# Optimization experiments

Hardware: AMD Instinct MI355X
Metric: run time of the kernel (lower is better)

## Reference

```python
import jax, jax.numpy as jnp
import numpy as np

K = 10           # polynomial order
N = 100000       # num nodes
E = 3200000      # num edges
F_IN = 512       # input feature dim
C = 64           # num classes


def setup_inputs() -> dict:
    key = jax.random.key(0)
    ks = jax.random.split(key, 6)
    x = jax.random.normal(ks[0], (N, F_IN), dtype=jnp.float32)
    edge_index = jax.random.randint(ks[1], (2, E), 0, N, dtype=jnp.int64)
    W = jax.random.normal(ks[2], (F_IN, C), dtype=jnp.float32) * (1.0 / np.sqrt(F_IN))
    b = jax.random.normal(ks[3], (C,), dtype=jnp.float32) * 0.01
    lap_coefs = jax.random.uniform(ks[4], (K + 1,), dtype=jnp.float32)
    mf_weights = jax.random.uniform(ks[5], (1, K + 1, C), dtype=jnp.float32)
    return {"x": x, "edge_index": edge_index, "W": W, "b": b,
            "lap_coefs": lap_coefs, "mf_weights": mf_weights}


def reference(x, edge_index, W, b, lap_coefs, mf_weights):
    row, col = edge_index[0], edge_index[1]
    # GCN norm without self-loops: deg over targets (col), sym normalization
    ones = jnp.ones((row.shape[0],), dtype=x.dtype)
    deg = jax.ops.segment_sum(ones, col, num_segments=N)
    dinv = jnp.where(deg > 0, jax.lax.rsqrt(jnp.maximum(deg, 1.0)), 1.0)
    norm = dinv[row] * dinv[col]  # [E]

    h = x @ W + b  # [N, C]  (dropout is identity in eval mode)

    def prop(hx):
        # out[i] = sum_{(j->i)} norm_e * hx[j]
        return jax.ops.segment_sum(norm[:, None] * hx[row], col, num_segments=N)

    outs = [h, prop(h)]
    for _ in range(2, K + 1):
        # P_n = Bn*P_{n-1} + Cn*P_{n-2} + An*prop(P_{n-1}), An=2, Bn=0, Cn=-1
        outs.append(2.0 * prop(outs[-1]) - outs[-2])

    # coef_upd='none' -> coefs used directly; P0 gets coef 1, P_i gets lap_coefs[i-1]
    coefs = jnp.concatenate([jnp.ones((1,), lap_coefs.dtype), lap_coefs[:K]])  # [K+1]
    stacked = jnp.stack(outs, axis=1)  # [N, K+1, C]
    ret = jnp.sum(stacked * coefs[None, :, None] * mf_weights, axis=1)  # [N, C]
    return jax.nn.log_softmax(ret, axis=-1)
```

## Files before the change

kernel.cpp:

```cpp
#include <hip/hip_runtime.h>

#define F_IN 512
#define C_DIM 64
#define BUCKET_BITS 9
#define EPB 2048

typedef __bf16 bf16x8 __attribute__((ext_vector_type(8)));
typedef float f32x4 __attribute__((ext_vector_type(4)));

__device__ inline unsigned bf_rne(float x) {
    unsigned u = __float_as_uint(x);
    u += 0x7fffu + ((u >> 16) & 1u);
    return u >> 16;
}
__device__ inline unsigned bfpack(float x, float y) {
    return bf_rne(x) | (bf_rne(y) << 16);
}
__device__ inline bf16x8 as_bf16x8(uint4 u) {
    bf16x8 v; __builtin_memcpy(&v, &u, 16); return v;
}

__global__ void bucket_count(const int* __restrict__ col, int* __restrict__ bkcnt, int E) {
    __shared__ int h[256];
    int t = threadIdx.x;
    h[t] = 0;
    __syncthreads();
    int base = blockIdx.x * 4096 + t * 4;
    #pragma unroll
    for (int j = 0; j < 4; ++j) {
        int e = base + j * 1024;
        if (e + 3 < E) {
            int4 c4 = *(const int4*)(col + e);
            atomicAdd(&h[c4.x >> BUCKET_BITS], 1);
            atomicAdd(&h[c4.y >> BUCKET_BITS], 1);
            atomicAdd(&h[c4.z >> BUCKET_BITS], 1);
            atomicAdd(&h[c4.w >> BUCKET_BITS], 1);
        } else if (e < E) {
            for (int q = e; q < E; ++q) atomicAdd(&h[col[q] >> BUCKET_BITS], 1);
        }
    }
    __syncthreads();
    if (h[t]) atomicAdd(&bkcnt[t], h[t]);
}

__global__ void bucket_scan(const int* __restrict__ bkcnt, int* __restrict__ bucketbase,
                            int NB, int E) {
    __shared__ int tmp[256];
    int t = threadIdx.x;
    int v = (t < NB) ? bkcnt[t] : 0;
    tmp[t] = v;
    __syncthreads();
    for (int off = 1; off < 256; off <<= 1) {
        int u = (t >= off) ? tmp[t - off] : 0;
        __syncthreads();
        tmp[t] += u;
        __syncthreads();
    }
    if (t < NB) bucketbase[t] = tmp[t] - v;
    if (t == 0) bucketbase[NB] = E;
}

__global__ void bucket_stage(const int* __restrict__ row, const int* __restrict__ col,
                             const int* __restrict__ bucketbase, int* __restrict__ bcnt2,
                             int2* __restrict__ staged, int E) {
    __shared__ int lcnt[256];
    __shared__ int lbase[256];
    int t = threadIdx.x;
    lcnt[t] = 0;
    __syncthreads();
    int base_e = blockIdx.x * EPB;
    int rr[8], cc[8], pk[8];
    #pragma unroll
    for (int j = 0; j < 8; ++j) {
        int e = base_e + j * 256 + t;
        pk[j] = -1;
        if (e < E) {
            rr[j] = row[e];
            cc[j] = col[e];
            int b = cc[j] >> BUCKET_BITS;
            int off = atomicAdd(&lcnt[b], 1);
            pk[j] = off | (b << 20);
        }
    }
    __syncthreads();
    lbase[t] = lcnt[t] ? atomicAdd(&bcnt2[t], lcnt[t]) : 0;
    __syncthreads();
    #pragma unroll
    for (int j = 0; j < 8; ++j) {
        if (pk[j] >= 0) {
            int b = pk[j] >> 20;
            int off = pk[j] & 0xFFFFF;
            int pos = bucketbase[b] + lbase[b] + off;
            staged[pos] = make_int2(rr[j], cc[j]);
        }
    }
}

__global__ void bucket_deg(const int2* __restrict__ staged, const int* __restrict__ bucketbase,
                           int* __restrict__ rowptr, float* __restrict__ dinv, int N, int E) {
    __shared__ int cnt[512];
    int t = threadIdx.x;
    int b = blockIdx.x;
    int beg = bucketbase[b];
    int end = bucketbase[b + 1];
    cnt[t] = 0;
    __syncthreads();
    for (int i = beg + t; i < end; i += 512)
        atomicAdd(&cnt[staged[i].y & 511], 1);
    __syncthreads();
    int v = cnt[t];
    for (int off = 1; off < 512; off <<= 1) {
        int u = (t >= off) ? cnt[t - off] : 0;
        __syncthreads();
        cnt[t] += u;
        __syncthreads();
    }
    int node = (b << BUCKET_BITS) + t;
    if (node < N) {
        rowptr[node] = beg + cnt[t] - v;
        dinv[node] = (v > 0) ? (1.0f / sqrtf((float)v)) : 1.0f;
    }
    if (b == 0 && t == 0) rowptr[N] = E;
}

__global__ void bucket_final(const int2* __restrict__ staged, const int* __restrict__ bucketbase,
                             const int* __restrict__ rowptr, const float* __restrict__ dinv,
                             int2* __restrict__ edges, int N) {
    __shared__ int lcnt[512];
    __shared__ int lrow[512];
    __shared__ float ldinv[512];
    int t = threadIdx.x;
    int b = blockIdx.x;
    int beg = bucketbase[b];
    int end = bucketbase[b + 1];
    int node = (b << BUCKET_BITS) + t;
    lcnt[t] = 0;
    lrow[t] = (node < N) ? rowptr[node] : 0;
    ldinv[t] = (node < N) ? dinv[node] : 1.0f;
    __syncthreads();
    for (int i = beg + t; i < end; i += 512) {
        int2 rc = staged[i];
        int cl = rc.y & 511;
        float nrm = dinv[rc.x] * ldinv[cl];
        int pos = lrow[cl] + atomicAdd(&lcnt[cl], 1);
        edges[pos] = make_int2(rc.x, __float_as_int(nrm));
    }
}

__global__ void wprep_kernel(const float* __restrict__ W,
                             uint4* __restrict__ whi, uint4* __restrict__ wlo) {
    int tid = blockIdx.x * 256 + threadIdx.x;
    int kslot = tid >> 8;
    int rem = tid & 255;
    int ct = rem >> 6;
    int l = rem & 63;
    int col = ct * 16 + (l & 15);
    int kbase = kslot * 32 + ((l >> 4) << 3);
    unsigned hbits[8], lbits[8];
    #pragma unroll
    for (int j = 0; j < 8; ++j) {
        float f = W[(size_t)(kbase + j) * C_DIM + col];
        unsigned h = bf_rne(f);
        hbits[j] = h;
        lbits[j] = bf_rne(f - __uint_as_float(h << 16));
    }
    whi[tid] = make_uint4(hbits[0] | (hbits[1] << 16), hbits[2] | (hbits[3] << 16),
                          hbits[4] | (hbits[5] << 16), hbits[6] | (hbits[7] << 16));
    wlo[tid] = make_uint4(lbits[0] | (lbits[1] << 16), lbits[2] | (lbits[3] << 16),
                          lbits[4] | (lbits[5] << 16), lbits[6] | (lbits[7] << 16));
}

__global__ __launch_bounds__(256) void gemm_mfma(const float4* __restrict__ x4,
                                                 const uint4* __restrict__ whi,
                                                 const uint4* __restrict__ wlo,
                                                 const float* __restrict__ bias,
                                                 uint4* __restrict__ hb, int N) {
    __shared__ float smem[8704];
    char* ahi = (char*)smem;
    char* alo = ahi + 16384;
    const int t = threadIdx.x;
    const int l = t & 63;
    const int wv = t >> 6;
    const int rowblk = blockIdx.x * 128;

    f32x4 acc[2][4];
    #pragma unroll
    for (int rt = 0; rt < 2; ++rt)
        #pragma unroll
        for (int ct = 0; ct < 4; ++ct) acc[rt][ct] = (f32x4){0.f, 0.f, 0.f, 0.f};

    for (int chunk = 0; chunk < 8; ++chunk) {
        #pragma unroll
        for (int i = 0; i < 4; ++i) {
            int idx = t + 256 * i;
            int r = idx >> 3, g = idx & 7;
            int grow = rowblk + r;
            float4 v0 = make_float4(0.f, 0.f, 0.f, 0.f), v1 = v0;
            if (grow < N) {
                const float4* p = x4 + (size_t)grow * (F_IN / 4) + chunk * 16 + g * 2;
                v0 = p[0]; v1 = p[1];
            }
            float f[8] = {v0.x, v0.y, v0.z, v0.w, v1.x, v1.y, v1.z, v1.w};
            unsigned hbits[8], lbits[8];
            #pragma unroll
            for (int j = 0; j < 8; ++j) {
                unsigned h = bf_rne(f[j]);
                hbits[j] = h;
                lbits[j] = bf_rne(f[j] - __uint_as_float(h << 16));
            }
            int off = r * 128 + ((g ^ (r & 7)) << 4);
            *(uint4*)(ahi + off) = make_uint4(hbits[0] | (hbits[1] << 16), hbits[2] | (hbits[3] << 16),
                                              hbits[4] | (hbits[5] << 16), hbits[6] | (hbits[7] << 16));
            *(uint4*)(alo + off) = make_uint4(lbits[0] | (lbits[1] << 16), lbits[2] | (lbits[3] << 16),
                                              lbits[4] | (lbits[5] << 16), lbits[6] | (lbits[7] << 16));
        }
        __syncthreads();
        uint4 AH[2][2], AL[2][2];
        #pragma unroll
        for (int rt = 0; rt < 2; ++rt) {
            int r = wv * 32 + rt * 16 + (l & 15);
            int rb = r * 128;
            int rx = r & 7;
            #pragma unroll
            for (int ks = 0; ks < 2; ++ks) {
                int gl = ks * 4 + (l >> 4);
                int off = rb + ((gl ^ rx) << 4);
                AH[rt][ks] = *(const uint4*)(ahi + off);
                AL[rt][ks] = *(const uint4*)(alo + off);
            }
        }
        #pragma unroll
        for (int ct = 0; ct < 4; ++ct) {
            int base = (chunk * 8 + ct) * 64 + l;
            uint4 BH0 = whi[base], BH1 = whi[base + 256];
            uint4 BL0 = wlo[base], BL1 = wlo[base + 256];
            #pragma unroll
            for (int rt = 0; rt < 2; ++rt) {
                f32x4 c = acc[rt][ct];
                c = __builtin_amdgcn_mfma_f32_16x16x32_bf16(as_bf16x8(AH[rt][0]), as_bf16x8(BH0), c, 0, 0, 0);
                c = __builtin_amdgcn_mfma_f32_16x16x32_bf16(as_bf16x8(AH[rt][1]), as_bf16x8(BH1), c, 0, 0, 0);
                c = __builtin_amdgcn_mfma_f32_16x16x32_bf16(as_bf16x8(AL[rt][0]), as_bf16x8(BH0), c, 0, 0, 0);
                c = __builtin_amdgcn_mfma_f32_16x16x32_bf16(as_bf16x8(AL[rt][1]), as_bf16x8(BH1), c, 0, 0, 0);
                c = __builtin_amdgcn_mfma_f32_16x16x32_bf16(as_bf16x8(AH[rt][0]), as_bf16x8(BL0), c, 0, 0, 0);
                c = __builtin_amdgcn_mfma_f32_16x16x32_bf16(as_bf16x8(AH[rt][1]), as_bf16x8(BL1), c, 0, 0, 0);
                acc[rt][ct] = c;
            }
        }
        __syncthreads();
    }
    float* ls = smem;
    #pragma unroll
    for (int rt = 0; rt < 2; ++rt) {
        int rbase = wv * 32 + rt * 16 + ((l >> 4) << 2);
        #pragma unroll
        for (int ct = 0; ct < 4; ++ct) {
            int col = ct * 16 + (l & 15);
            float bb = bias[col];
            #pragma unroll
            for (int q = 0; q < 4; ++q)
                ls[(rbase + q) * 68 + col] = acc[rt][ct][q] + bb;
        }
    }
    __syncthreads();
    #pragma unroll
    for (int i = 0; i < 4; ++i) {
        int idx = t + 256 * i;
        int r = idx >> 3, lc = idx & 7;
        int grow = rowblk + r;
        if (grow < N) {
            const float* p = ls + r * 68 + lc * 8;
            float4 A = *(const float4*)p;
            float4 Bv = *(const float4*)(p + 4);
            uint4 nb;
            nb.x = bfpack(A.x, A.y);
            nb.y = bfpack(A.z, A.w);
            nb.z = bfpack(Bv.x, Bv.y);
            nb.w = bfpack(Bv.z, Bv.w);
            hb[(size_t)grow * 8 + lc] = nb;
        }
    }
}

__global__ void prop_kernel(const int* __restrict__ rowptr, const int2* __restrict__ edges,
                            const uint4* __restrict__ Hb, const uint4* Pold,
                            uint4* Pout, float4* ret, const float* lap,
                            const float4* mf4, int k, int mode, int N) {
    int gtid = blockIdx.x * blockDim.x + threadIdx.x;
    int node = gtid >> 3;
    int lc = gtid & 7;
    if (node >= N) return;
    int beg = rowptr[node];
    int end = rowptr[node + 1];
    float a0 = 0.f, a1 = 0.f, a2 = 0.f, a3 = 0.f, a4 = 0.f, a5 = 0.f, a6 = 0.f, a7 = 0.f;

#define EDGE_FMA(SRC, WB) do { \
        float w_ = __int_as_float(WB); \
        uint4 u_ = Hb[(size_t)(SRC) * 8 + lc]; \
        a0 = fmaf(w_, __uint_as_float(u_.x << 16), a0); \
        a1 = fmaf(w_, __uint_as_float(u_.x & 0xffff0000u), a1); \
        a2 = fmaf(w_, __uint_as_float(u_.y << 16), a2); \
        a3 = fmaf(w_, __uint_as_float(u_.y & 0xffff0000u), a3); \
        a4 = fmaf(w_, __uint_as_float(u_.z << 16), a4); \
        a5 = fmaf(w_, __uint_as_float(u_.z & 0xffff0000u), a5); \
        a6 = fmaf(w_, __uint_as_float(u_.w << 16), a6); \
        a7 = fmaf(w_, __uint_as_float(u_.w & 0xffff0000u), a7); \
    } while (0)

    int e = beg;
    if ((e & 1) && e < end) {
        int2 d = edges[e];
        EDGE_FMA(d.x, d.y);
        ++e;
    }
    for (; e + 4 <= end; e += 4) {
        int4 p0v = ((const int4*)edges)[e >> 1];
        int4 p1v = ((const int4*)edges)[(e >> 1) + 1];
        EDGE_FMA(p0v.x, p0v.y);
        EDGE_FMA(p0v.z, p0v.w);
        EDGE_FMA(p1v.x, p1v.y);
        EDGE_FMA(p1v.z, p1v.w);
    }
    for (; e < end; ++e) {
        int2 d = edges[e];
        EDGE_FMA(d.x, d.y);
    }
#undef EDGE_FMA

    size_t ib = (size_t)node * 8 + lc;
    float p0, p1, p2, p3, p4, p5, p6, p7;
    if (mode == 0) {
        p0 = a0; p1 = a1; p2 = a2; p3 = a3; p4 = a4; p5 = a5; p6 = a6; p7 = a7;
    } else {
        uint4 ob = Pold[ib];
        p0 = 2.f * a0 - __uint_as_float(ob.x << 16);
        p1 = 2.f * a1 - __uint_as_float(ob.x & 0xffff0000u);
        p2 = 2.f * a2 - __uint_as_float(ob.y << 16);
        p3 = 2.f * a3 - __uint_as_float(ob.y & 0xffff0000u);
        p4 = 2.f * a4 - __uint_as_float(ob.z << 16);
        p5 = 2.f * a5 - __uint_as_float(ob.z & 0xffff0000u);
        p6 = 2.f * a6 - __uint_as_float(ob.w << 16);
        p7 = 2.f * a7 - __uint_as_float(ob.w & 0xffff0000u);
    }
    uint4 nb;
    nb.x = bfpack(p0, p1);
    nb.y = bfpack(p2, p3);
    nb.z = bfpack(p4, p5);
    nb.w = bfpack(p6, p7);
    Pout[ib] = nb;

    if (ret) {
        float lw = lap[k - 1];
        size_t i16 = (size_t)node * 16 + lc * 2;
        float4 m0 = mf4[k * 16 + lc * 2];
        float4 m1 = mf4[k * 16 + lc * 2 + 1];
        float4 r0 = ret[i16];
        float4 r1 = ret[i16 + 1];
        r0.x = fmaf(lw * m0.x, p0, r0.x);
        r0.y = fmaf(lw * m0.y, p1, r0.y);
        r0.z = fmaf(lw * m0.z, p2, r0.z);
        r0.w = fmaf(lw * m0.w, p3, r0.w);
        r1.x = fmaf(lw * m1.x, p4, r1.x);
        r1.y = fmaf(lw * m1.y, p5, r1.y);
        r1.z = fmaf(lw * m1.z, p6, r1.z);
        r1.w = fmaf(lw * m1.w, p7, r1.w);
        ret[i16] = r0;
        ret[i16 + 1] = r1;
    }
}

__global__ void combine_kernel(const uint4* __restrict__ hb, const uint4* __restrict__ Pall,
                               const float* __restrict__ lap, const float* __restrict__ mf,
                               float4* __restrict__ ret, int Kp, int N) {
    __shared__ float smf[1024];
    __shared__ float slap[32];
    int t = threadIdx.x;
    int nmf = (Kp + 1) * 64;
    for (int i = t; i < nmf; i += 256) smf[i] = mf[i];
    if (t < Kp) slap[t] = lap[t];
    __syncthreads();
    int g = blockIdx.x * 256 + t;
    int node = g >> 3, lc = g & 7;
    if (node >= N) return;
    size_t off = (size_t)node * 8 + lc;
    uint4 u = hb[off];
    const float* m0 = smf + lc * 8;
    float a0 = __uint_as_float(u.x << 16) * m0[0];
    float a1 = __uint_as_float(u.x & 0xffff0000u) * m0[1];
    float a2 = __uint_as_float(u.y << 16) * m0[2];
    float a3 = __uint_as_float(u.y & 0xffff0000u) * m0[3];
    float a4 = __uint_as_float(u.z << 16) * m0[4];
    float a5 = __uint_as_float(u.z & 0xffff0000u) * m0[5];
    float a6 = __uint_as_float(u.w << 16) * m0[6];
    float a7 = __uint_as_float(u.w & 0xffff0000u) * m0[7];
    size_t stride = (size_t)N * 8;
    for (int k = 1; k <= Kp; ++k) {
        uint4 p = Pall[(size_t)(k - 1) * stride + off];
        float cw = slap[k - 1];
        const float* mk = smf + k * 64 + lc * 8;
        a0 = fmaf(cw * mk[0], __uint_as_float(p.x << 16), a0);
        a1 = fmaf(cw * mk[1], __uint_as_float(p.x & 0xffff0000u), a1);
        a2 = fmaf(cw * mk[2], __uint_as_float(p.y << 16), a2);
        a3 = fmaf(cw * mk[3], __uint_as_float(p.y & 0xffff0000u), a3);
        a4 = fmaf(cw * mk[4], __uint_as_float(p.z << 16), a4);
        a5 = fmaf(cw * mk[5], __uint_as_float(p.z & 0xffff0000u), a5);
        a6 = fmaf(cw * mk[6], __uint_as_float(p.w << 16), a6);
        a7 = fmaf(cw * mk[7], __uint_as_float(p.w & 0xffff0000u), a7);
    }
    float m = fmaxf(fmaxf(fmaxf(a0, a1), fmaxf(a2, a3)), fmaxf(fmaxf(a4, a5), fmaxf(a6, a7)));
    for (int o = 1; o < 8; o <<= 1) m = fmaxf(m, __shfl_xor(m, o, 8));
    float s = __expf(a0 - m) + __expf(a1 - m) + __expf(a2 - m) + __expf(a3 - m)
            + __expf(a4 - m) + __expf(a5 - m) + __expf(a6 - m) + __expf(a7 - m);
    for (int o = 1; o < 8; o <<= 1) s += __shfl_xor(s, o, 8);
    float lg = logf(s) + m;
    ret[(size_t)node * 16 + lc * 2]     = make_float4(a0 - lg, a1 - lg, a2 - lg, a3 - lg);
    ret[(size_t)node * 16 + lc * 2 + 1] = make_float4(a4 - lg, a5 - lg, a6 - lg, a7 - lg);
}

__global__ void p0ret_kernel(const uint4* __restrict__ hb, float4* __restrict__ ret,
                             const float4* __restrict__ mf4, int N) {
    int g = blockIdx.x * 256 + threadIdx.x;
    int node = g >> 3, lc = g & 7;
    if (node >= N) return;
    uint4 u = hb[(size_t)node * 8 + lc];
    float4 m0 = mf4[lc * 2], m1 = mf4[lc * 2 + 1];
    float4 r0 = make_float4(__uint_as_float(u.x << 16) * m0.x,
                            __uint_as_float(u.x & 0xffff0000u) * m0.y,
                            __uint_as_float(u.y << 16) * m0.z,
                            __uint_as_float(u.y & 0xffff0000u) * m0.w);
    float4 r1 = make_float4(__uint_as_float(u.z << 16) * m1.x,
                            __uint_as_float(u.z & 0xffff0000u) * m1.y,
                            __uint_as_float(u.w << 16) * m1.z,
                            __uint_as_float(u.w & 0xffff0000u) * m1.w);
    ret[(size_t)node * 16 + lc * 2] = r0;
    ret[(size_t)node * 16 + lc * 2 + 1] = r1;
}

__global__ void lsm_kernel(float* __restrict__ ret, int N) {
    int wid = (blockIdx.x * blockDim.x + threadIdx.x) >> 6;
    int c = threadIdx.x & 63;
    if (wid >= N) return;
    size_t idx = (size_t)wid * C_DIM + c;
    float v = ret[idx];
    float m = v;
    for (int off = 32; off; off >>= 1) m = fmaxf(m, __shfl_xor(m, off, 64));
    float ex = __expf(v - m);
    float s = ex;
    for (int off = 32; off; off >>= 1) s += __shfl_xor(s, off, 64);
    ret[idx] = (v - m) - logf(s);
}

extern "C" void kernel_launch(void* const* d_in, const int* in_sizes, int n_in,
                              void* d_out, int out_size, void* d_ws, size_t ws_size,
                              hipStream_t stream) {
    const float* x   = (const float*)d_in[0];
    const int*   ei  = (const int*)d_in[1];
    const float* W   = (const float*)d_in[2];
    const float* b   = (const float*)d_in[3];
    const float* lap = (const float*)d_in[4];
    const float* mf  = (const float*)d_in[5];
    float* ret = (float*)d_out;

    const int C = in_sizes[3];
    const int FIN = in_sizes[2] / C;
    const int N = in_sizes[0] / FIN;
    const int E = in_sizes[1] / 2;
    const int K = in_sizes[4] - 1;
    const int* rowi = ei;
    const int* coli = ei + E;
    const int NB = (N + (1 << BUCKET_BITS) - 1) >> BUCKET_BITS;

    char* w = (char*)d_ws;
    auto alloc = [&](size_t bytes) {
        void* p = (void*)w;
        w += (bytes + 255) & ~(size_t)255;
        return p;
    };
    int*   rowptr = (int*)alloc((size_t)(N + 1) * 4);
    float* dinv   = (float*)alloc((size_t)N * 4);
    int*   bkcnt  = (int*)alloc(1024);
    int*   bucketbase = (int*)alloc(4096);
    int*   bcnt2  = (int*)alloc(1024);
    uint4* whi    = (uint4*)alloc(65536);
    uint4* wlo    = (uint4*)alloc(65536);
    int2*  edges  = (int2*)alloc((size_t)E * 8);
    uint4* hb     = (uint4*)alloc((size_t)N * 128);

    const size_t slab = (size_t)N * 128;
    size_t used = (size_t)(w - (char*)d_ws);
    bool lazy = (ws_size > used) && ((ws_size - used) >= (size_t)K * slab);

    uint4* Pall = nullptr;
    uint4* pb = nullptr;
    int2* staged;
    if (lazy) {
        Pall = (uint4*)alloc((size_t)K * slab);
        staged = (int2*)Pall;
    } else {
        pb = (uint4*)alloc(slab);
        staged = (int2*)hb;
    }

    hipMemsetAsync(bkcnt, 0, 1024, stream);
    hipMemsetAsync(bcnt2, 0, 1024, stream);

    bucket_count<<<(E + 4095) / 4096, 256, 0, stream>>>(coli, bkcnt, E);
    bucket_scan<<<1, 256, 0, stream>>>(bkcnt, bucketbase, NB, E);
    bucket_stage<<<(E + EPB - 1) / EPB, 256, 0, stream>>>(rowi, coli, bucketbase, bcnt2,
                                                          staged, E);
    bucket_deg<<<NB, 512, 0, stream>>>(staged, bucketbase, rowptr, dinv, N, E);
    bucket_final<<<NB, 512, 0, stream>>>(staged, bucketbase, rowptr, dinv, edges, N);

    wprep_kernel<<<16, 256, 0, stream>>>(W, whi, wlo);
    gemm_mfma<<<(N + 127) / 128, 256, 0, stream>>>((const float4*)x, whi, wlo, b, hb, N);

    int pgrid = (N * 8 + 255) / 256;
    if (lazy) {
        prop_kernel<<<pgrid, 256, 0, stream>>>(rowptr, edges, hb, Pall, Pall,
                                               nullptr, nullptr, nullptr, 1, 0, N);
        for (int k2 = 2; k2 <= K; ++k2) {
            const uint4* src  = Pall + (size_t)(k2 - 2) * N * 8;
            const uint4* pold = (k2 == 2) ? hb : Pall + (size_t)(k2 - 3) * N * 8;
            uint4* out = Pall + (size_t)(k2 - 1) * N * 8;
            prop_kernel<<<pgrid, 256, 0, stream>>>(rowptr, edges, src, pold, out,
                                                   nullptr, nullptr, nullptr, k2, 1, N);
        }
        combine_kernel<<<pgrid, 256, 0, stream>>>(hb, Pall, lap, mf, (float4*)ret, K, N);
    } else {
        p0ret_kernel<<<pgrid, 256, 0, stream>>>(hb, (float4*)ret, (const float4*)mf, N);
        prop_kernel<<<pgrid, 256, 0, stream>>>(rowptr, edges, hb, pb, pb, (float4*)ret,
                                               lap, (const float4*)mf, 1, 0, N);
        uint4* gat = pb;
        uint4* st  = hb;
        for (int k2 = 2; k2 <= K; ++k2) {
            prop_kernel<<<pgrid, 256, 0, stream>>>(rowptr, edges, gat, st, st, (float4*)ret,
                                                   lap, (const float4*)mf, k2, 1, N);
            uint4* t2 = gat; gat = st; st = t2;
        }
        lsm_kernel<<<((size_t)N * 64 + 255) / 256, 256, 0, stream>>>(ret, N);
    }
}
```

Before: 1.040 ms.

## Use one wavefront per node in lazy propagation path with shuffle reduction

Adds prop2_kernel, which assigns a full 64-lane wavefront to each node: 8 groups of 8 lanes each gather a different edge, four edges per group are fetched per iteration, and a cross-group xor-shuffle reduction combines the partial sums. The lazy path now launches this kernel for all propagation steps. The goal is more memory-level parallelism per node on the random gathers and less load imbalance from uneven degrees. It costs wasted lanes when a node has few edges (average degree 32), plus shuffle overhead. The old prop_kernel's vectorized edge loop is also simplified to a scalar loop, which may slow the non-lazy path.

```diff
diff --git a/kernel.cpp b/kernel.cpp
--- a/kernel.cpp
+++ b/kernel.cpp
@@ -281,6 +281,88 @@
     }
 }
 
+__global__ __launch_bounds__(256) void prop2_kernel(const int* __restrict__ rowptr,
+                                                    const int2* __restrict__ edges,
+                                                    const uint4* __restrict__ Hb,
+                                                    const uint4* __restrict__ Pold,
+                                                    uint4* __restrict__ Pout,
+                                                    int mode, int N) {
+    int wid = (blockIdx.x * 256 + threadIdx.x) >> 6;
+    if (wid >= N) return;
+    int l = threadIdx.x & 63;
+    int g = l >> 3;
+    int lc = l & 7;
+    int beg = rowptr[wid];
+    int count = rowptr[wid + 1] - beg;
+
+    float a0 = 0.f, a1 = 0.f, a2 = 0.f, a3 = 0.f, a4 = 0.f, a5 = 0.f, a6 = 0.f, a7 = 0.f;
+
+    for (int base = 0; base < count; base += 32) {
+        int2 d[4];
+        float wv[4];
+        #pragma unroll
+        for (int s = 0; s < 4; ++s) {
+            int eidx = base + s * 8 + g;
+            bool v = eidx < count;
+            d[s] = edges[beg + (v ? eidx : 0)];
+            wv[s] = v ? __int_as_float(d[s].y) : 0.f;
+        }
+        uint4 u[4];
+        #pragma unroll
+        for (int s = 0; s < 4; ++s)
+            u[s] = Hb[(size_t)d[s].x * 8 + lc];
+        #pragma unroll
+        for (int s = 0; s < 4; ++s) {
+            float w_ = wv[s];
+            uint4 u_ = u[s];
+            a0 = fmaf(w_, __uint_as_float(u_.x << 16), a0);
+            a1 = fmaf(w_, __uint_as_float(u_.x & 0xffff0000u), a1);
+            a2 = fmaf(w_, __uint_as_float(u_.y << 16), a2);
+            a3 = fmaf(w_, __uint_as_float(u_.y & 0xffff0000u), a3);
+            a4 = fmaf(w_, __uint_as_float(u_.z << 16), a4);
+            a5 = fmaf(w_, __uint_as_float(u_.z & 0xffff0000u), a5);
+            a6 = fmaf(w_, __uint_as_float(u_.w << 16), a6);
+            a7 = fmaf(w_, __uint_as_float(u_.w & 0xffff0000u), a7);
+        }
+    }
+
+    #pragma unroll
+    for (int off = 8; off <= 32; off <<= 1) {
+        a0 += __shfl_xor(a0, off, 64);
+        a1 += __shfl_xor(a1, off, 64);
+        a2 += __shfl_xor(a2, off, 64);
+        a3 += __shfl_xor(a3, off, 64);
+        a4 += __shfl_xor(a4, off, 64);
+        a5 += __shfl_xor(a5, off, 64);
+        a6 += __shfl_xor(a6, off, 64);
+        a7 += __shfl_xor(a7, off, 64);
+    }
+
+    if (l < 8) {
+        size_t ib = (size_t)wid * 8 + lc;
+        float p0, p1, p2, p3, p4, p5, p6, p7;
+        if (mode == 0) {
+            p0 = a0; p1 = a1; p2 = a2; p3 = a3; p4 = a4; p5 = a5; p6 = a6; p7 = a7;
+        } else {
+            uint4 ob = Pold[ib];
+            p0 = 2.f * a0 - __uint_as_float(ob.x << 16);
+            p1 = 2.f * a1 - __uint_as_float(ob.x & 0xffff0000u);
+            p2 = 2.f * a2 - __uint_as_float(ob.y << 16);
+            p3 = 2.f * a3 - __uint_as_float(ob.y & 0xffff0000u);
+            p4 = 2.f * a4 - __uint_as_float(ob.z << 16);
+            p5 = 2.f * a5 - __uint_as_float(ob.z & 0xffff0000u);
+            p6 = 2.f * a6 - __uint_as_float(ob.w << 16);
+            p7 = 2.f * a7 - __uint_as_float(ob.w & 0xffff0000u);
+        }
+        uint4 nb;
+        nb.x = bfpack(p0, p1);
+        nb.y = bfpack(p2, p3);
+        nb.z = bfpack(p4, p5);
+        nb.w = bfpack(p6, p7);
+        Pout[ib] = nb;
+    }
+}
+
 __global__ void prop_kernel(const int* __restrict__ rowptr, const int2* __restrict__ edges,
                             const uint4* __restrict__ Hb, const uint4* Pold,
                             uint4* Pout, float4* ret, const float* lap,
@@ -306,23 +388,9 @@
         a7 = fmaf(w_, __uint_as_float(u_.w & 0xffff0000u), a7); \
     } while (0)
 
-    int e = beg;
-    if ((e & 1) && e < end) {
-        int2 d = edges[e];
-        EDGE_FMA(d.x, d.y);
-        ++e;
-    }
-    for (; e + 4 <= end; e += 4) {
-        int4 p0v = ((const int4*)edges)[e >> 1];
-        int4 p1v = ((const int4*)edges)[(e >> 1) + 1];
-        EDGE_FMA(p0v.x, p0v.y);
-        EDGE_FMA(p0v.z, p0v.w);
-        EDGE_FMA(p1v.x, p1v.y);
-        EDGE_FMA(p1v.z, p1v.w);
-    }
-    for (; e < end; ++e) {
-        int2 d = edges[e];
-        EDGE_FMA(d.x, d.y);
+    for (int e = beg; e < end; ++e) {
+        int2 dd = edges[e];
+        EDGE_FMA(dd.x, dd.y);
     }
 #undef EDGE_FMA
 
@@ -513,19 +581,19 @@
     wprep_kernel<<<16, 256, 0, stream>>>(W, whi, wlo);
     gemm_mfma<<<(N + 127) / 128, 256, 0, stream>>>((const float4*)x, whi, wlo, b, hb, N);
 
-    int pgrid = (N * 8 + 255) / 256;
     if (lazy) {
-        prop_kernel<<<pgrid, 256, 0, stream>>>(rowptr, edges, hb, Pall, Pall,
-                                               nullptr, nullptr, nullptr, 1, 0, N);
+        int pgrid2 = (N + 3) / 4;
+        prop2_kernel<<<pgrid2, 256, 0, stream>>>(rowptr, edges, hb, Pall, Pall, 0, N);
         for (int k2 = 2; k2 <= K; ++k2) {
             const uint4* src  = Pall + (size_t)(k2 - 2) * N * 8;
             const uint4* pold = (k2 == 2) ? hb : Pall + (size_t)(k2 - 3) * N * 8;
             uint4* out = Pall + (size_t)(k2 - 1) * N * 8;
-            prop_kernel<<<pgrid, 256, 0, stream>>>(rowptr, edges, src, pold, out,
-                                                   nullptr, nullptr, nullptr, k2, 1, N);
-        }
+            prop2_kernel<<<pgrid2, 256, 0, stream>>>(rowptr, edges, src, pold, out, 1, N);
+        }
+        int pgrid = (N * 8 + 255) / 256;
         combine_kernel<<<pgrid, 256, 0, stream>>>(hb, Pall, lap, mf, (float4*)ret, K, N);
     } else {
+        int pgrid = (N * 8 + 255) / 256;
         p0ret_kernel<<<pgrid, 256, 0, stream>>>(hb, (float4*)ret, (const float4*)mf, N);
         prop_kernel<<<pgrid, 256, 0, stream>>>(rowptr, edges, hb, pb, pb, (float4*)ret,
                                                lap, (const float4*)mf, 1, 0, N);
```

Result: faster. 999.4 us (-3.9%).

## Sort nodes by degree for load-balanced propagation kernel

Applied to the files above, without the earlier changes.

Adds a counting sort of nodes by in-degree (histogram, scan, scatter) that builds a permutation, and a new prop3_kernel that processes nodes in that order so each wavefront handles nodes of similar degree. This targets divergence from uneven edge-loop lengths within a wave. In exchange it adds three small kernels, an extra indirection per thread, and scattered output writes that break row locality. The bucket memset is widened so the relocated counters are zeroed together.

```diff
diff --git a/kernel.cpp b/kernel.cpp
--- a/kernel.cpp
+++ b/kernel.cpp
@@ -145,6 +145,56 @@
         int pos = lrow[cl] + atomicAdd(&lcnt[cl], 1);
         edges[pos] = make_int2(rc.x, __float_as_int(nrm));
     }
+}
+
+__global__ void sort_hist(const int* __restrict__ rowptr, int* __restrict__ ghist, int N) {
+    __shared__ int h[256];
+    int t = threadIdx.x;
+    h[t] = 0;
+    __syncthreads();
+    int i = blockIdx.x * 256 + t;
+    if (i < N) {
+        int d = rowptr[i + 1] - rowptr[i];
+        if (d > 255) d = 255;
+        atomicAdd(&h[d], 1);
+    }
+    __syncthreads();
+    if (h[t]) atomicAdd(&ghist[t], h[t]);
+}
+
+__global__ void sort_scan(const int* __restrict__ ghist, int* __restrict__ binbase) {
+    __shared__ int tmp[256];
+    int t = threadIdx.x;
+    int v = ghist[t];
+    tmp[t] = v;
+    __syncthreads();
+    for (int off = 1; off < 256; off <<= 1) {
+        int u = (t >= off) ? tmp[t - off] : 0;
+        __syncthreads();
+        tmp[t] += u;
+        __syncthreads();
+    }
+    binbase[t] = tmp[t] - v;
+}
+
+__global__ void sort_scatter(const int* __restrict__ rowptr, const int* __restrict__ binbase,
+                             int* __restrict__ gcnt, int* __restrict__ perm, int N) {
+    __shared__ int lcnt[256];
+    __shared__ int lbase[256];
+    int t = threadIdx.x;
+    lcnt[t] = 0;
+    __syncthreads();
+    int i = blockIdx.x * 256 + t;
+    int d = 0, off = 0;
+    if (i < N) {
+        d = rowptr[i + 1] - rowptr[i];
+        if (d > 255) d = 255;
+        off = atomicAdd(&lcnt[d], 1);
+    }
+    __syncthreads();
+    lbase[t] = lcnt[t] ? atomicAdd(&gcnt[t], lcnt[t]) : 0;
+    __syncthreads();
+    if (i < N) perm[binbase[d] + lbase[d] + off] = i;
 }
 
 __global__ void wprep_kernel(const float* __restrict__ W,
@@ -281,14 +331,18 @@
     }
 }
 
-__global__ void prop_kernel(const int* __restrict__ rowptr, const int2* __restrict__ edges,
-                            const uint4* __restrict__ Hb, const uint4* Pold,
-                            uint4* Pout, float4* ret, const float* lap,
-                            const float4* mf4, int k, int mode, int N) {
+__global__ __launch_bounds__(256) void prop3_kernel(const int* __restrict__ rowptr,
+                                                    const int2* __restrict__ edges,
+                                                    const int* __restrict__ perm,
+                                                    const uint4* __restrict__ Hb,
+                                                    const uint4* __restrict__ Pold,
+                                                    uint4* __restrict__ Pout,
+                                                    int mode, int N) {
     int gtid = blockIdx.x * blockDim.x + threadIdx.x;
-    int node = gtid >> 3;
+    int gi = gtid >> 3;
     int lc = gtid & 7;
-    if (node >= N) return;
+    if (gi >= N) return;
+    int node = perm[gi];
     int beg = rowptr[node];
     int end = rowptr[node + 1];
     float a0 = 0.f, a1 = 0.f, a2 = 0.f, a3 = 0.f, a4 = 0.f, a5 = 0.f, a6 = 0.f, a7 = 0.f;
@@ -323,6 +377,60 @@
     for (; e < end; ++e) {
         int2 d = edges[e];
         EDGE_FMA(d.x, d.y);
+    }
+#undef EDGE_FMA
+
+    size_t ib = (size_t)node * 8 + lc;
+    float p0, p1, p2, p3, p4, p5, p6, p7;
+    if (mode == 0) {
+        p0 = a0; p1 = a1; p2 = a2; p3 = a3; p4 = a4; p5 = a5; p6 = a6; p7 = a7;
+    } else {
+        uint4 ob = Pold[ib];
+        p0 = 2.f * a0 - __uint_as_float(ob.x << 16);
+        p1 = 2.f * a1 - __uint_as_float(ob.x & 0xffff0000u);
+        p2 = 2.f * a2 - __uint_as_float(ob.y << 16);
+        p3 = 2.f * a3 - __uint_as_float(ob.y & 0xffff0000u);
+        p4 = 2.f * a4 - __uint_as_float(ob.z << 16);
+        p5 = 2.f * a5 - __uint_as_float(ob.z & 0xffff0000u);
+        p6 = 2.f * a6 - __uint_as_float(ob.w << 16);
+        p7 = 2.f * a7 - __uint_as_float(ob.w & 0xffff0000u);
+    }
+    uint4 nb;
+    nb.x = bfpack(p0, p1);
+    nb.y = bfpack(p2, p3);
+    nb.z = bfpack(p4, p5);
+    nb.w = bfpack(p6, p7);
+    Pout[ib] = nb;
+}
+
+__global__ void prop_kernel(const int* __restrict__ rowptr, const int2* __restrict__ edges,
+                            const uint4* __restrict__ Hb, const uint4* Pold,
+                            uint4* Pout, float4* ret, const float* lap,
+                            const float4* mf4, int k, int mode, int N) {
+    int gtid = blockIdx.x * blockDim.x + threadIdx.x;
+    int node = gtid >> 3;
+    int lc = gtid & 7;
+    if (node >= N) return;
+    int beg = rowptr[node];
+    int end = rowptr[node + 1];
+    float a0 = 0.f, a1 = 0.f, a2 = 0.f, a3 = 0.f, a4 = 0.f, a5 = 0.f, a6 = 0.f, a7 = 0.f;
+
+#define EDGE_FMA(SRC, WB) do { \
+        float w_ = __int_as_float(WB); \
+        uint4 u_ = Hb[(size_t)(SRC) * 8 + lc]; \
+        a0 = fmaf(w_, __uint_as_float(u_.x << 16), a0); \
+        a1 = fmaf(w_, __uint_as_float(u_.x & 0xffff0000u), a1); \
+        a2 = fmaf(w_, __uint_as_float(u_.y << 16), a2); \
+        a3 = fmaf(w_, __uint_as_float(u_.y & 0xffff0000u), a3); \
+        a4 = fmaf(w_, __uint_as_float(u_.z << 16), a4); \
+        a5 = fmaf(w_, __uint_as_float(u_.z & 0xffff0000u), a5); \
+        a6 = fmaf(w_, __uint_as_float(u_.w << 16), a6); \
+        a7 = fmaf(w_, __uint_as_float(u_.w & 0xffff0000u), a7); \
+    } while (0)
+
+    for (int e = beg; e < end; ++e) {
+        int2 dd = edges[e];
+        EDGE_FMA(dd.x, dd.y);
     }
 #undef EDGE_FMA
 
@@ -477,9 +585,13 @@
     };
     int*   rowptr = (int*)alloc((size_t)(N + 1) * 4);
     float* dinv   = (float*)alloc((size_t)N * 4);
+    int*   perm   = (int*)alloc((size_t)N * 4);
     int*   bkcnt  = (int*)alloc(1024);
+    int*   bcnt2  = (int*)alloc(1024);
+    int*   shist  = (int*)alloc(1024);
+    int*   sgcnt  = (int*)alloc(1024);
     int*   bucketbase = (int*)alloc(4096);
-    int*   bcnt2  = (int*)alloc(1024);
+    int*   binbase    = (int*)alloc(1024);
     uint4* whi    = (uint4*)alloc(65536);
     uint4* wlo    = (uint4*)alloc(65536);
     int2*  edges  = (int2*)alloc((size_t)E * 8);
@@ -500,8 +612,7 @@
         staged = (int2*)hb;
     }
 
-    hipMemsetAsync(bkcnt, 0, 1024, stream);
-    hipMemsetAsync(bcnt2, 0, 1024, stream);
+    hipMemsetAsync(bkcnt, 0, 4096, stream);
 
     bucket_count<<<(E + 4095) / 4096, 256, 0, stream>>>(coli, bkcnt, E);
     bucket_scan<<<1, 256, 0, stream>>>(bkcnt, bucketbase, NB, E);
@@ -510,19 +621,22 @@
     bucket_deg<<<NB, 512, 0, stream>>>(staged, bucketbase, rowptr, dinv, N, E);
     bucket_final<<<NB, 512, 0, stream>>>(staged, bucketbase, rowptr, dinv, edges, N);
 
+    int sgrid = (N + 255) / 256;
+    sort_hist<<<sgrid, 256, 0, stream>>>(rowptr, shist, N);
+    sort_scan<<<1, 256, 0, stream>>>(shist, binbase);
+    sort_scatter<<<sgrid, 256, 0, stream>>>(rowptr, binbase, sgcnt, perm, N);
+
     wprep_kernel<<<16, 256, 0, stream>>>(W, whi, wlo);
     gemm_mfma<<<(N + 127) / 128, 256, 0, stream>>>((const float4*)x, whi, wlo, b, hb, N);
 
     int pgrid = (N * 8 + 255) / 256;
     if (lazy) {
-        prop_kernel<<<pgrid, 256, 0, stream>>>(rowptr, edges, hb, Pall, Pall,
-                                               nullptr, nullptr, nullptr, 1, 0, N);
+        prop3_kernel<<<pgrid, 256, 0, stream>>>(rowptr, edges, perm, hb, Pall, Pall, 0, N);
         for (int k2 = 2; k2 <= K; ++k2) {
             const uint4* src  = Pall + (size_t)(k2 - 2) * N * 8;
             const uint4* pold = (k2 == 2) ? hb : Pall + (size_t)(k2 - 3) * N * 8;
             uint4* out = Pall + (size_t)(k2 - 1) * N * 8;
-            prop_kernel<<<pgrid, 256, 0, stream>>>(rowptr, edges, src, pold, out,
-                                                   nullptr, nullptr, nullptr, k2, 1, N);
+            prop3_kernel<<<pgrid, 256, 0, stream>>>(rowptr, edges, perm, src, pold, out, 1, N);
         }
         combine_kernel<<<pgrid, 256, 0, stream>>>(hb, Pall, lap, mf, (float4*)ret, K, N);
     } else {
```

Result: slower. 1.065 ms (+2.4%).
